# Kernel tuning notes

Measured on AMD Instinct MI355X. Metric: run time of the kernel, lower is better.

Reference implementation:

```python
import jax, jax.numpy as jnp
import numpy as np

V = 100000
E = 1600000
BN_EPS = 1e-5


def spmm(edge_index, vals, X):
    # X: (V, Cin, B); sparse L @ X via scatter-add. y[r] += w * X[c]
    rows, cols = edge_index[0], edge_index[1]
    return jnp.zeros_like(X).at[rows].add(vals[:, None, None] * X[cols])


def cheb_conv(x, edge_index, vals, w, b=None):
    # x: (B, Cin, V), w: (K, Cin, Cout) -> (B, Cout, V)
    K = w.shape[0]
    x0 = jnp.transpose(x, (2, 1, 0))  # (V, Cin, B)
    xs = [x0]
    if K > 1:
        x1 = spmm(edge_index, vals, x0)
        xs.append(x1)
        for _ in range(2, K):
            x2 = 2.0 * spmm(edge_index, vals, x1) - x0
            xs.append(x2)
            x0, x1 = x1, x2
    xk = jnp.stack(xs)  # (K, V, Cin, B)
    out = jnp.einsum('kvcb,kco->bov', xk, w)
    if b is not None:
        out = out + b[None, :, None]
    return out


def batch_norm(x, g, b):
    # training-mode BatchNorm1d on (B, C, V): stats over (B, V), biased var
    m = jnp.mean(x, axis=(0, 2), keepdims=True)
    v = jnp.var(x, axis=(0, 2), keepdims=True)
    return g[None, :, None] * (x - m) * jax.lax.rsqrt(v + BN_EPS) + b[None, :, None]


def setup_inputs() -> dict:
    key = jax.random.key(0)
    ks = jax.random.split(key, 8)
    x = jax.random.normal(ks[0], (4, 32, V), dtype=jnp.float32)
    edge_index = jax.random.randint(ks[1], (2, E), 0, V, dtype=jnp.int32)
    # small values keep the K=4 Chebyshev recursion well-scaled
    lap_vals = 0.1 * jax.random.normal(ks[2], (E,), dtype=jnp.float32)
    def w(k, K, cin, cout):
        s = 1.0 / np.sqrt(K * cin)
        return s * jax.random.normal(k, (K, cin, cout), dtype=jnp.float32)
    return {
        'x': x, 'edge_index': edge_index, 'lap_vals': lap_vals,
        'in_bn_g': jnp.ones((32,), jnp.float32), 'in_bn_b': jnp.zeros((32,), jnp.float32),
        'in_w': w(ks[3], 4, 32, 64), 'in_b': jnp.zeros((64,), jnp.float32),
        'h0_bn_g': jnp.ones((64,), jnp.float32), 'h0_bn_b': jnp.zeros((64,), jnp.float32),
        'h0_w': w(ks[4], 4, 64, 64), 'h0_b': jnp.zeros((64,), jnp.float32),
        'h1_bn_g': jnp.ones((64,), jnp.float32), 'h1_bn_b': jnp.zeros((64,), jnp.float32),
        'h1_w': w(ks[5], 4, 64, 32), 'h1_b': jnp.zeros((32,), jnp.float32),
    }


def reference(x, edge_index, lap_vals, in_bn_g, in_bn_b, in_w, in_b,
              h0_bn_g, h0_bn_b, h0_w, h0_b, h1_bn_g, h1_bn_b, h1_w, h1_b):
    xn = batch_norm(x, in_bn_g, in_bn_b)
    out = cheb_conv(xn, edge_index, lap_vals, in_w, in_b)
    # hidden layer 0
    out = jax.nn.relu(out)
    out = batch_norm(out, h0_bn_g, h0_bn_b)
    out = cheb_conv(out, edge_index, lap_vals, h0_w, h0_b)
    # hidden layer 1
    out = jax.nn.relu(out)
    out = batch_norm(out, h1_bn_g, h1_bn_b)
    out = cheb_conv(out, edge_index, lap_vals, h1_w, h1_b)
    # in_channels == out_channels -> Identity shortcut on the BN'ed input
    return jax.nn.relu(out + xn)
```

## Files before the change

### kernel.cpp

```cpp
#include <hip/hip_runtime.h>
#include <cstdint>
#include <cstddef>

#define VN 100000
#define EN 1600000
static constexpr float BN_EPS_F = 1e-5f;
static constexpr float INV_N = 1.0f / 400000.0f;

using short8 = __attribute__((ext_vector_type(8))) short;
using f32x4  = __attribute__((ext_vector_type(4))) float;

__device__ __forceinline__ float bf_lo(unsigned int p) {
  return __builtin_bit_cast(float, p << 16);
}
__device__ __forceinline__ float bf_hi(unsigned int p) {
  return __builtin_bit_cast(float, p & 0xffff0000u);
}
__device__ __forceinline__ float bf1(unsigned short u) {
  return __builtin_bit_cast(float, ((unsigned int)u) << 16);
}
__device__ __forceinline__ unsigned short f2bf(float f) {
  unsigned int x = __builtin_bit_cast(unsigned int, f);
  x += 0x7fffu + ((x >> 16) & 1u);
  return (unsigned short)(x >> 16);
}
__device__ __forceinline__ unsigned int pack2(float a, float b) {
  return (unsigned int)f2bf(a) | ((unsigned int)f2bf(b) << 16);
}

__global__ __launch_bounds__(256) void stats_x_kernel(const float* __restrict__ x,
                                                      float* __restrict__ stats) {
  const int p = blockIdx.x & 127;
  const int chunk = blockIdx.x >> 7;
  const int c = p & 31, b = p >> 5;
  const float* base = x + ((size_t)b * 32 + c) * VN + chunk * 12500;
  float s = 0.f, s2 = 0.f;
  for (int i = threadIdx.x; i < 12500; i += 256) {
    float v = base[i];
    s += v; s2 += v * v;
  }
  __shared__ float r1[256], r2[256];
  r1[threadIdx.x] = s; r2[threadIdx.x] = s2;
  __syncthreads();
  for (int off = 128; off > 0; off >>= 1) {
    if (threadIdx.x < off) {
      r1[threadIdx.x] += r1[threadIdx.x + off];
      r2[threadIdx.x] += r2[threadIdx.x + off];
    }
    __syncthreads();
  }
  if (threadIdx.x == 0) {
    atomicAdd(&stats[c], r1[0]);
    atomicAdd(&stats[64 + c], r2[0]);
  }
}

__global__ void finalize_stats_kernel(float* __restrict__ stats,
                                      const float* __restrict__ g,
                                      const float* __restrict__ beta, int C) {
  int c = threadIdx.x;
  if (c < C) {
    float m = stats[c] * INV_N;
    float var = stats[64 + c] * INV_N - m * m;
    float sc = g[c] * rsqrtf(var + BN_EPS_F);
    stats[128 + c] = sc;
    stats[192 + c] = beta[c] - m * sc;
  }
}

__global__ __launch_bounds__(128) void bn_transpose_kernel(const float* __restrict__ x,
                                                           const float* __restrict__ stats,
                                                           unsigned short* __restrict__ xn) {
  const int tid = threadIdx.x;
  const int b = tid >> 5, c = tid & 31;
  const int v0 = blockIdx.x * 64;
  const float sc = stats[128 + c], sh = stats[192 + c];
  const float* src = x + ((size_t)b * 32 + c) * VN;
  for (int i = 0; i < 64; i++) {
    int v = v0 + i;
    if (v < VN) xn[(size_t)v * 128 + tid] = f2bf(sc * src[v] + sh);
  }
}

__global__ __launch_bounds__(256) void pack_wb_kernel(const float* __restrict__ W,
                                                      unsigned short* __restrict__ Wb,
                                                      int Cin, int Cout) {
  const int i = blockIdx.x * 256 + threadIdx.x;
  const int KC = Cin >> 5, T = Cout >> 4;
  const int tot = 4 * KC * T * 512;
  if (i >= tot) return;
  const int j = i & 7;
  const int l = (i >> 3) & 63;
  const int rem = i >> 9;
  const int t = rem % T;
  const int kc = (rem / T) % KC;
  const int k = rem / (T * KC);
  const int c = kc * 32 + (l >> 4) * 8 + j;
  const int o = t * 16 + (l & 15);
  Wb[i] = f2bf(W[((size_t)k * Cin + c) * Cout + o]);
}

__global__ __launch_bounds__(256) void hist_kernel(const int* __restrict__ rows,
                                                   int* __restrict__ cnt) {
  int i = blockIdx.x * blockDim.x + threadIdx.x;
  const int stride = gridDim.x * blockDim.x;
  for (; i < EN; i += stride) atomicAdd(&cnt[rows[i]], 1);
}

__global__ __launch_bounds__(256) void scan1_kernel(const int* __restrict__ cnt,
                                                    int* __restrict__ rp,
                                                    int* __restrict__ chunkSums) {
  __shared__ int sh[256];
  const int t = threadIdx.x;
  const int base = blockIdx.x * 2048 + t * 8;
  int vals[8]; int tot = 0;
#pragma unroll
  for (int i = 0; i < 8; i++) {
    int idx = base + i;
    int v = (idx < VN) ? cnt[idx] : 0;
    vals[i] = v; tot += v;
  }
  sh[t] = tot;
  __syncthreads();
  for (int off = 1; off < 256; off <<= 1) {
    int v = (t >= off) ? sh[t - off] : 0;
    __syncthreads();
    sh[t] += v;
    __syncthreads();
  }
  int run = sh[t] - tot;
#pragma unroll
  for (int i = 0; i < 8; i++) {
    int idx = base + i;
    if (idx < VN) rp[idx] = run;
    run += vals[i];
  }
  if (t == 255) chunkSums[blockIdx.x] = sh[255];
}

__global__ void scan2_kernel(const int* __restrict__ chunkSums,
                             int* __restrict__ chunkOff,
                             int* __restrict__ rp, int nChunks) {
  if (threadIdx.x == 0 && blockIdx.x == 0) {
    int off = 0;
    for (int j = 0; j < nChunks; j++) { chunkOff[j] = off; off += chunkSums[j]; }
    rp[VN] = off;
  }
}

__global__ __launch_bounds__(256) void scan3_kernel(int* __restrict__ rp,
                                                    const int* __restrict__ chunkOff,
                                                    int* __restrict__ fill) {
  int i = blockIdx.x * 256 + threadIdx.x;
  if (i < VN) {
    int v = rp[i] + chunkOff[i >> 11];
    rp[i] = v;
    fill[i] = v;
  }
}

__global__ __launch_bounds__(256) void fill_kernel(const int* __restrict__ rows,
                                                   const int* __restrict__ cols,
                                                   const float* __restrict__ lap,
                                                   int* __restrict__ fill,
                                                   int* __restrict__ cols_s,
                                                   float* __restrict__ vals_s) {
  int i = blockIdx.x * blockDim.x + threadIdx.x;
  const int stride = gridDim.x * blockDim.x;
  for (; i < EN; i += stride) {
    int r = rows[i];
    int pos = atomicAdd(&fill[r], 1);
    cols_s[pos] = cols[i];
    vals_s[pos] = lap[i];
  }
}

template <int EPL, bool CHEB>
__global__ __launch_bounds__(256, 8) void spmm_kernel(const int* __restrict__ rp,
                                                   const int* __restrict__ cs,
                                                   const float* __restrict__ vs,
                                                   const unsigned short* __restrict__ X, int XS,
                                                   const unsigned short* __restrict__ P, int PS,
                                                   unsigned short* __restrict__ Y, int YS) {
  const int lane = threadIdx.x & 63;
  const int row = blockIdx.x * 4 + (threadIdx.x >> 6);
  const int start = rp[row], end = rp[row + 1];
  float acc[EPL];
#pragma unroll
  for (int j = 0; j < EPL; j++) acc[j] = 0.f;
  int e = start;
  for (; e + 4 <= end; e += 4) {
    const int c0 = cs[e], c1 = cs[e + 1], c2 = cs[e + 2], c3 = cs[e + 3];
    const float w0 = vs[e], w1 = vs[e + 1], w2 = vs[e + 2], w3 = vs[e + 3];
    if constexpr (EPL == 4) {
      const uint2 q0 = *reinterpret_cast<const uint2*>(X + (size_t)c0 * XS + lane * 4);
      const uint2 q1 = *reinterpret_cast<const uint2*>(X + (size_t)c1 * XS + lane * 4);
      const uint2 q2 = *reinterpret_cast<const uint2*>(X + (size_t)c2 * XS + lane * 4);
      const uint2 q3 = *reinterpret_cast<const uint2*>(X + (size_t)c3 * XS + lane * 4);
      acc[0] += w0 * bf_lo(q0.x) + w1 * bf_lo(q1.x) + w2 * bf_lo(q2.x) + w3 * bf_lo(q3.x);
      acc[1] += w0 * bf_hi(q0.x) + w1 * bf_hi(q1.x) + w2 * bf_hi(q2.x) + w3 * bf_hi(q3.x);
      acc[2] += w0 * bf_lo(q0.y) + w1 * bf_lo(q1.y) + w2 * bf_lo(q2.y) + w3 * bf_lo(q3.y);
      acc[3] += w0 * bf_hi(q0.y) + w1 * bf_hi(q1.y) + w2 * bf_hi(q2.y) + w3 * bf_hi(q3.y);
    } else {
      const unsigned int q0 = *reinterpret_cast<const unsigned int*>(X + (size_t)c0 * XS + lane * 2);
      const unsigned int q1 = *reinterpret_cast<const unsigned int*>(X + (size_t)c1 * XS + lane * 2);
      const unsigned int q2 = *reinterpret_cast<const unsigned int*>(X + (size_t)c2 * XS + lane * 2);
      const unsigned int q3 = *reinterpret_cast<const unsigned int*>(X + (size_t)c3 * XS + lane * 2);
      acc[0] += w0 * bf_lo(q0) + w1 * bf_lo(q1) + w2 * bf_lo(q2) + w3 * bf_lo(q3);
      acc[1] += w0 * bf_hi(q0) + w1 * bf_hi(q1) + w2 * bf_hi(q2) + w3 * bf_hi(q3);
    }
  }
  for (; e < end; e++) {
    const int c0 = cs[e];
    const float w0 = vs[e];
    if constexpr (EPL == 4) {
      const uint2 q0 = *reinterpret_cast<const uint2*>(X + (size_t)c0 * XS + lane * 4);
      acc[0] += w0 * bf_lo(q0.x);
      acc[1] += w0 * bf_hi(q0.x);
      acc[2] += w0 * bf_lo(q0.y);
      acc[3] += w0 * bf_hi(q0.y);
    } else {
      const unsigned int q0 = *reinterpret_cast<const unsigned int*>(X + (size_t)c0 * XS + lane * 2);
      acc[0] += w0 * bf_lo(q0);
      acc[1] += w0 * bf_hi(q0);
    }
  }
  if constexpr (EPL == 4) {
    if constexpr (CHEB) {
      const uint2 p = *reinterpret_cast<const uint2*>(P + (size_t)row * PS + lane * 4);
      acc[0] = 2.f * acc[0] - bf_lo(p.x);
      acc[1] = 2.f * acc[1] - bf_hi(p.x);
      acc[2] = 2.f * acc[2] - bf_lo(p.y);
      acc[3] = 2.f * acc[3] - bf_hi(p.y);
    }
    uint2 r;
    r.x = pack2(acc[0], acc[1]);
    r.y = pack2(acc[2], acc[3]);
    *reinterpret_cast<uint2*>(Y + (size_t)row * YS + lane * 4) = r;
  } else {
    if constexpr (CHEB) {
      const unsigned int p = *reinterpret_cast<const unsigned int*>(P + (size_t)row * PS + lane * 2);
      acc[0] = 2.f * acc[0] - bf_lo(p);
      acc[1] = 2.f * acc[1] - bf_hi(p);
    }
    *reinterpret_cast<unsigned int*>(Y + (size_t)row * YS + lane * 2) = pack2(acc[0], acc[1]);
  }
}

template <int Cin, int Cout, int X0S>
__global__ __launch_bounds__(256, 8) void fused_cheb_kernel(const int* __restrict__ rp,
                                                         const int* __restrict__ cs,
                                                         const float* __restrict__ vs,
                                                         const unsigned short* __restrict__ X0,
                                                         unsigned short* __restrict__ A,
                                                         const unsigned short* __restrict__ B,
                                                         const unsigned short* __restrict__ Wb,
                                                         const float* __restrict__ Bias) {
  constexpr int EPL = Cin * 4 / 64;
  constexpr int ROWSH = Cin * 4;
  __shared__ unsigned short t3s[4 * ROWSH];
  const int lane = threadIdx.x & 63;
  const int wv = threadIdx.x >> 6;
  const int row0 = blockIdx.x * 4;
  const int row = row0 + wv;

  float g[EPL];
#pragma unroll
  for (int j = 0; j < EPL; j++) g[j] = 0.f;
  const int start = rp[row], end = rp[row + 1];
  int e = start;
  for (; e + 4 <= end; e += 4) {
    const int c0 = cs[e], c1 = cs[e + 1], c2 = cs[e + 2], c3 = cs[e + 3];
    const float w0 = vs[e], w1 = vs[e + 1], w2 = vs[e + 2], w3 = vs[e + 3];
    if constexpr (EPL == 4) {
      const uint2 q0 = *reinterpret_cast<const uint2*>(B + (size_t)c0 * 256 + lane * 4);
      const uint2 q1 = *reinterpret_cast<const uint2*>(B + (size_t)c1 * 256 + lane * 4);
      const uint2 q2 = *reinterpret_cast<const uint2*>(B + (size_t)c2 * 256 + lane * 4);
      const uint2 q3 = *reinterpret_cast<const uint2*>(B + (size_t)c3 * 256 + lane * 4);
      g[0] += w0 * bf_lo(q0.x) + w1 * bf_lo(q1.x) + w2 * bf_lo(q2.x) + w3 * bf_lo(q3.x);
      g[1] += w0 * bf_hi(q0.x) + w1 * bf_hi(q1.x) + w2 * bf_hi(q2.x) + w3 * bf_hi(q3.x);
      g[2] += w0 * bf_lo(q0.y) + w1 * bf_lo(q1.y) + w2 * bf_lo(q2.y) + w3 * bf_lo(q3.y);
      g[3] += w0 * bf_hi(q0.y) + w1 * bf_hi(q1.y) + w2 * bf_hi(q2.y) + w3 * bf_hi(q3.y);
    } else {
      const unsigned int q0 = *reinterpret_cast<const unsigned int*>(B + (size_t)c0 * 256 + lane * 2);
      const unsigned int q1 = *reinterpret_cast<const unsigned int*>(B + (size_t)c1 * 256 + lane * 2);
      const unsigned int q2 = *reinterpret_cast<const unsigned int*>(B + (size_t)c2 * 256 + lane * 2);
      const unsigned int q3 = *reinterpret_cast<const unsigned int*>(B + (size_t)c3 * 256 + lane * 2);
      g[0] += w0 * bf_lo(q0) + w1 * bf_lo(q1) + w2 * bf_lo(q2) + w3 * bf_lo(q3);
      g[1] += w0 * bf_hi(q0) + w1 * bf_hi(q1) + w2 * bf_hi(q2) + w3 * bf_hi(q3);
    }
  }
  for (; e < end; e++) {
    const int c0 = cs[e];
    const float w0 = vs[e];
    if constexpr (EPL == 4) {
      const uint2 q0 = *reinterpret_cast<const uint2*>(B + (size_t)c0 * 256 + lane * 4);
      g[0] += w0 * bf_lo(q0.x);
      g[1] += w0 * bf_hi(q0.x);
      g[2] += w0 * bf_lo(q0.y);
      g[3] += w0 * bf_hi(q0.y);
    } else {
      const unsigned int q0 = *reinterpret_cast<const unsigned int*>(B + (size_t)c0 * 256 + lane * 2);
      g[0] += w0 * bf_lo(q0);
      g[1] += w0 * bf_hi(q0);
    }
  }
  {
    unsigned int* tw = reinterpret_cast<unsigned int*>(t3s + wv * ROWSH);
    if constexpr (EPL == 4) {
      const uint2 p = *reinterpret_cast<const uint2*>(A + (size_t)row * 256 + lane * 4);
      tw[lane * 2]     = pack2(2.f * g[0] - bf_lo(p.x), 2.f * g[1] - bf_hi(p.x));
      tw[lane * 2 + 1] = pack2(2.f * g[2] - bf_lo(p.y), 2.f * g[3] - bf_hi(p.y));
    } else {
      const unsigned int p = *reinterpret_cast<const unsigned int*>(A + (size_t)row * 256 + lane * 2);
      tw[lane] = pack2(2.f * g[0] - bf_lo(p), 2.f * g[1] - bf_hi(p));
    }
  }
  __syncthreads();

  constexpr int KC = Cin / 32;
  constexpr int T = Cout / 16;
  const int col = lane & 15, quad = lane >> 4;
  const int t = wv % T;
  const int ar = col >> 2, ab = col & 3;

  const unsigned short* xap[3];
  xap[0] = X0 + (size_t)(row0 + ar) * X0S + ab * Cin + quad * 8;
  xap[1] = A  + (size_t)(row0 + ar) * 256 + ab * Cin + quad * 8;
  xap[2] = B  + (size_t)(row0 + ar) * 256 + ab * Cin + quad * 8;
  const unsigned short* wb = Wb + (size_t)t * 512 + lane * 8;

  f32x4 acc = {0.f, 0.f, 0.f, 0.f};
#pragma unroll
  for (int k = 0; k < 3; k++) {
#pragma unroll
    for (int kc = 0; kc < KC; kc++) {
      const short8 af = *reinterpret_cast<const short8*>(xap[k] + kc * 32);
      const short8 bf = *reinterpret_cast<const short8*>(wb + (size_t)(k * KC + kc) * T * 512);
      acc = __builtin_amdgcn_mfma_f32_16x16x32_bf16(af, bf, acc, 0, 0, 0);
    }
  }
#pragma unroll
  for (int kc = 0; kc < KC; kc++) {
    const short8 af = *reinterpret_cast<const short8*>(&t3s[ar * ROWSH + ab * Cin + kc * 32 + quad * 8]);
    const short8 bf = *reinterpret_cast<const short8*>(wb + (size_t)(3 * KC + kc) * T * 512);
    acc = __builtin_amdgcn_mfma_f32_16x16x32_bf16(af, bf, acc, 0, 0, 0);
  }
  __syncthreads();

  if (T == 4 || wv < 2) {
    const int og = t * 16 + col;
    const float bs = Bias[og];
#pragma unroll
    for (int r = 0; r < 4; r++) {
      A[(size_t)(row0 + quad) * 256 + r * Cout + og] = f2bf(acc[r] + bs);
    }
  }
}

__global__ __launch_bounds__(256) void stats_out_kernel(const unsigned short* __restrict__ SRC,
                                                        float* __restrict__ stats) {
  const int tid = threadIdx.x;
  const int per = (VN + gridDim.x - 1) / gridDim.x;
  const int v0 = blockIdx.x * per;
  const int v1 = (v0 + per < VN) ? (v0 + per) : VN;
  float s = 0.f, s2 = 0.f;
  for (int v = v0; v < v1; v++) {
    float val = bf1(SRC[(size_t)v * 256 + tid]);
    val = fmaxf(val, 0.f);
    s += val; s2 += val * val;
  }
  __shared__ float r1[256], r2[256];
  r1[tid] = s; r2[tid] = s2;
  __syncthreads();
  if (tid < 64) {
    float a = r1[tid] + r1[tid + 64] + r1[tid + 128] + r1[tid + 192];
    float b = r2[tid] + r2[tid + 64] + r2[tid + 128] + r2[tid + 192];
    atomicAdd(&stats[tid], a);
    atomicAdd(&stats[64 + tid], b);
  }
}

__global__ __launch_bounds__(256) void bn_relu_kernel(const unsigned short* __restrict__ SRC,
                                                      const float* __restrict__ stats,
                                                      unsigned short* __restrict__ DST) {
  const int i = blockIdx.x * 256 + threadIdx.x;
  const int w = i & 63;
  const int o0 = (w & 15) * 4;
  const float4 sc4 = *reinterpret_cast<const float4*>(stats + 128 + o0);
  const float4 sh4 = *reinterpret_cast<const float4*>(stats + 192 + o0);
  const uint2 q = reinterpret_cast<const uint2*>(SRC)[i];
  float a = fmaxf(bf_lo(q.x), 0.f);
  float b = fmaxf(bf_hi(q.x), 0.f);
  float c = fmaxf(bf_lo(q.y), 0.f);
  float d = fmaxf(bf_hi(q.y), 0.f);
  uint2 r;
  r.x = pack2(a * sc4.x + sh4.x, b * sc4.y + sh4.y);
  r.y = pack2(c * sc4.z + sh4.z, d * sc4.w + sh4.w);
  reinterpret_cast<uint2*>(DST)[i] = r;
}

__global__ __launch_bounds__(256) void final_kernel(const unsigned short* __restrict__ SRC,
                                                    const unsigned short* __restrict__ xn,
                                                    float* __restrict__ out) {
  const int lane = threadIdx.x & 63;
  const int grp = threadIdx.x >> 6;
  const int v = blockIdx.x * 64 + lane;
  if (v >= VN) return;
  for (int ob = grp; ob < 128; ob += 4) {
    float val = bf1(SRC[(size_t)v * 256 + ob]) + bf1(xn[(size_t)v * 128 + ob]);
    val = fmaxf(val, 0.f);
    out[(size_t)ob * VN + v] = val;
  }
}

static constexpr size_t align_up(size_t x) { return (x + 255) & ~(size_t)255; }
static constexpr size_t OFF_RP    = 0;
static constexpr size_t OFF_FILL  = align_up(OFF_RP + (size_t)(VN + 1) * 4);
static constexpr size_t OFF_CHS   = align_up(OFF_FILL + (size_t)VN * 4);
static constexpr size_t OFF_CHO   = align_up(OFF_CHS + 256);
static constexpr size_t OFF_STATS = align_up(OFF_CHO + 256);
static constexpr size_t OFF_WP    = align_up(OFF_STATS + 1024);
static constexpr size_t OFF_CS    = align_up(OFF_WP + 32768 * 2);
static constexpr size_t OFF_VS    = align_up(OFF_CS + (size_t)EN * 4);
static constexpr size_t OFF_XN    = align_up(OFF_VS + (size_t)EN * 4);
static constexpr size_t OFF_XL    = align_up(OFF_XN + (size_t)VN * 128 * 2);
static constexpr size_t OFF_A     = align_up(OFF_XL + (size_t)VN * 256 * 2);
static constexpr size_t OFF_B     = align_up(OFF_A + (size_t)VN * 256 * 2);
static constexpr size_t OFF_END   = OFF_B + (size_t)VN * 256 * 2;

extern "C" void kernel_launch(void* const* d_in, const int* in_sizes, int n_in,
                              void* d_out, int out_size, void* d_ws, size_t ws_size,
                              hipStream_t stream) {
  if (ws_size < OFF_END) return;

  const float* x       = (const float*)d_in[0];
  const int*   rows    = (const int*)d_in[1];
  const int*   cols    = rows + EN;
  const float* lap     = (const float*)d_in[2];
  const float* in_bn_g = (const float*)d_in[3];
  const float* in_bn_b = (const float*)d_in[4];
  const float* in_w    = (const float*)d_in[5];
  const float* in_b    = (const float*)d_in[6];
  const float* h0_bn_g = (const float*)d_in[7];
  const float* h0_bn_b = (const float*)d_in[8];
  const float* h0_w    = (const float*)d_in[9];
  const float* h0_b    = (const float*)d_in[10];
  const float* h1_bn_g = (const float*)d_in[11];
  const float* h1_bn_b = (const float*)d_in[12];
  const float* h1_w    = (const float*)d_in[13];
  const float* h1_b    = (const float*)d_in[14];
  float* outp = (float*)d_out;

  char* ws = (char*)d_ws;
  int*   rp     = (int*)(ws + OFF_RP);
  int*   fill   = (int*)(ws + OFF_FILL);
  int*   chS    = (int*)(ws + OFF_CHS);
  int*   chO    = (int*)(ws + OFF_CHO);
  float* stats  = (float*)(ws + OFF_STATS);
  unsigned short* wbIn = (unsigned short*)(ws + OFF_WP);
  unsigned short* wbH0 = wbIn + 8192;
  unsigned short* wbH1 = wbH0 + 16384;
  int*   cs     = (int*)(ws + OFF_CS);
  float* vs     = (float*)(ws + OFF_VS);
  unsigned short* xn = (unsigned short*)(ws + OFF_XN);
  unsigned short* XL = (unsigned short*)(ws + OFF_XL);
  unsigned short* A  = (unsigned short*)(ws + OFF_A);
  unsigned short* B  = (unsigned short*)(ws + OFF_B);

  const int nChunks = (VN + 2047) / 2048;

  pack_wb_kernel<<<32, 256, 0, stream>>>(in_w, wbIn, 32, 64);
  pack_wb_kernel<<<64, 256, 0, stream>>>(h0_w, wbH0, 64, 64);
  pack_wb_kernel<<<32, 256, 0, stream>>>(h1_w, wbH1, 64, 32);

  hipMemsetAsync(stats, 0, 1024, stream);
  stats_x_kernel<<<1024, 256, 0, stream>>>(x, stats);
  finalize_stats_kernel<<<1, 64, 0, stream>>>(stats, in_bn_g, in_bn_b, 32);
  bn_transpose_kernel<<<1563, 128, 0, stream>>>(x, stats, xn);

  hipMemsetAsync(fill, 0, (size_t)VN * 4, stream);
  hist_kernel<<<2048, 256, 0, stream>>>(rows, fill);
  scan1_kernel<<<nChunks, 256, 0, stream>>>(fill, rp, chS);
  scan2_kernel<<<1, 64, 0, stream>>>(chS, chO, rp, nChunks);
  scan3_kernel<<<(VN + 255) / 256, 256, 0, stream>>>(rp, chO, fill);
  fill_kernel<<<2048, 256, 0, stream>>>(rows, cols, lap, fill, cs, vs);

  spmm_kernel<2, false><<<VN / 4, 256, 0, stream>>>(rp, cs, vs, xn, 128, nullptr, 0, A, 256);
  spmm_kernel<2, true ><<<VN / 4, 256, 0, stream>>>(rp, cs, vs, A, 256, xn, 128, B, 256);
  fused_cheb_kernel<32, 64, 128><<<VN / 4, 256, 0, stream>>>(rp, cs, vs, xn, A, B, wbIn, in_b);
  hipMemsetAsync(stats, 0, 1024, stream);
  stats_out_kernel<<<256, 256, 0, stream>>>(A, stats);
  finalize_stats_kernel<<<1, 64, 0, stream>>>(stats, h0_bn_g, h0_bn_b, 64);
  bn_relu_kernel<<<VN * 64 / 256, 256, 0, stream>>>(A, stats, XL);

  spmm_kernel<4, false><<<VN / 4, 256, 0, stream>>>(rp, cs, vs, XL, 256, nullptr, 0, A, 256);
  spmm_kernel<4, true ><<<VN / 4, 256, 0, stream>>>(rp, cs, vs, A, 256, XL, 256, B, 256);
  fused_cheb_kernel<64, 64, 256><<<VN / 4, 256, 0, stream>>>(rp, cs, vs, XL, A, B, wbH0, h0_b);
  hipMemsetAsync(stats, 0, 1024, stream);
  stats_out_kernel<<<256, 256, 0, stream>>>(A, stats);
  finalize_stats_kernel<<<1, 64, 0, stream>>>(stats, h1_bn_g, h1_bn_b, 64);
  bn_relu_kernel<<<VN * 64 / 256, 256, 0, stream>>>(A, stats, XL);

  spmm_kernel<4, false><<<VN / 4, 256, 0, stream>>>(rp, cs, vs, XL, 256, nullptr, 0, A, 256);
  spmm_kernel<4, true ><<<VN / 4, 256, 0, stream>>>(rp, cs, vs, A, 256, XL, 256, B, 256);
  fused_cheb_kernel<64, 32, 256><<<VN / 4, 256, 0, stream>>>(rp, cs, vs, XL, A, B, wbH1, h1_b);

  final_kernel<<<1563, 256, 0, stream>>>(A, xn, outp);
}
```

Measured before the change: 1.806 ms.

## Apply last-layer weights before propagation and use Clenshaw recurrence on narrower features

For the final Chebyshev layer (64 in, 32 out channels), a new MFMA kernel first projects the input with each of the four weight slices, giving four 32-channel tensors z0..z3. The Chebyshev sum is then evaluated with a Clenshaw backward recurrence, built from three sparse multiplies on 128-element rows instead of 256-element rows. The goal is to halve the bytes gathered per edge in the last layer's sparse passes, which are bound by memory traffic. In exchange it adds a separate GEMM pass, extra reads of the z tensors, and bf16 rounding at different points in the recurrence. The A and B buffers now have to sit next to each other in the workspace.

Measured after the change: 1.637 ms. -9.3%, faster.

```diff
diff --git a/kernel.cpp b/kernel.cpp
--- a/kernel.cpp
+++ b/kernel.cpp
@@ -175,12 +175,13 @@
   }
 }
 
-template <int EPL, bool CHEB>
+template <int EPL, int MODE>
 __global__ __launch_bounds__(256, 8) void spmm_kernel(const int* __restrict__ rp,
                                                    const int* __restrict__ cs,
                                                    const float* __restrict__ vs,
                                                    const unsigned short* __restrict__ X, int XS,
                                                    const unsigned short* __restrict__ P, int PS,
+                                                   const unsigned short* __restrict__ Q, int QS,
                                                    unsigned short* __restrict__ Y, int YS) {
   const int lane = threadIdx.x & 63;
   const int row = blockIdx.x * 4 + (threadIdx.x >> 6);
@@ -226,24 +227,40 @@
     }
   }
   if constexpr (EPL == 4) {
-    if constexpr (CHEB) {
+    float r0 = acc[0], r1 = acc[1], r2 = acc[2], r3 = acc[3];
+    if constexpr (MODE == 1) {
       const uint2 p = *reinterpret_cast<const uint2*>(P + (size_t)row * PS + lane * 4);
-      acc[0] = 2.f * acc[0] - bf_lo(p.x);
-      acc[1] = 2.f * acc[1] - bf_hi(p.x);
-      acc[2] = 2.f * acc[2] - bf_lo(p.y);
-      acc[3] = 2.f * acc[3] - bf_hi(p.y);
+      r0 = 2.f * r0 - bf_lo(p.x);
+      r1 = 2.f * r1 - bf_hi(p.x);
+      r2 = 2.f * r2 - bf_lo(p.y);
+      r3 = 2.f * r3 - bf_hi(p.y);
     }
     uint2 r;
-    r.x = pack2(acc[0], acc[1]);
-    r.y = pack2(acc[2], acc[3]);
+    r.x = pack2(r0, r1);
+    r.y = pack2(r2, r3);
     *reinterpret_cast<uint2*>(Y + (size_t)row * YS + lane * 4) = r;
   } else {
-    if constexpr (CHEB) {
+    float r0 = acc[0], r1 = acc[1];
+    if constexpr (MODE == 1) {
       const unsigned int p = *reinterpret_cast<const unsigned int*>(P + (size_t)row * PS + lane * 2);
-      acc[0] = 2.f * acc[0] - bf_lo(p);
-      acc[1] = 2.f * acc[1] - bf_hi(p);
-    }
-    *reinterpret_cast<unsigned int*>(Y + (size_t)row * YS + lane * 2) = pack2(acc[0], acc[1]);
+      r0 = 2.f * r0 - bf_lo(p);
+      r1 = 2.f * r1 - bf_hi(p);
+    } else if constexpr (MODE == 2) {
+      const unsigned int p = *reinterpret_cast<const unsigned int*>(P + (size_t)row * PS + lane * 2);
+      r0 = 2.f * r0 + bf_lo(p);
+      r1 = 2.f * r1 + bf_hi(p);
+    } else if constexpr (MODE == 3) {
+      const unsigned int p = *reinterpret_cast<const unsigned int*>(P + (size_t)row * PS + lane * 2);
+      const unsigned int qq = *reinterpret_cast<const unsigned int*>(Q + (size_t)row * QS + lane * 2);
+      r0 = 2.f * r0 - bf_lo(qq) + bf_lo(p);
+      r1 = 2.f * r1 - bf_hi(qq) + bf_hi(p);
+    } else if constexpr (MODE == 4) {
+      const unsigned int p = *reinterpret_cast<const unsigned int*>(P + (size_t)row * PS + lane * 2);
+      const unsigned int qq = *reinterpret_cast<const unsigned int*>(Q + (size_t)row * QS + lane * 2);
+      r0 = r0 - bf_lo(qq) + bf_lo(p);
+      r1 = r1 - bf_hi(qq) + bf_hi(p);
+    }
+    *reinterpret_cast<unsigned int*>(Y + (size_t)row * YS + lane * 2) = pack2(r0, r1);
   }
 }
 
@@ -358,6 +375,36 @@
   }
 }
 
+__global__ __launch_bounds__(256, 8) void gemm_z_kernel(const unsigned short* __restrict__ XL,
+                                                        const unsigned short* __restrict__ Wb,
+                                                        const float* __restrict__ Bias,
+                                                        unsigned short* __restrict__ Z) {
+  const int lane = threadIdx.x & 63;
+  const int wv = threadIdx.x >> 6;
+  const int row0 = blockIdx.x * 4;
+  const int col = lane & 15, quad = lane >> 4;
+  const int ar = col >> 2, ab = col & 3;
+  const unsigned short* xa = XL + (size_t)(row0 + ar) * 256 + ab * 64 + quad * 8;
+  const unsigned short* wb = Wb + (size_t)wv * 4 * 512 + lane * 8;
+  unsigned short* zr = Z + (size_t)wv * VN * 128;
+#pragma unroll
+  for (int t = 0; t < 2; t++) {
+    f32x4 acc = {0.f, 0.f, 0.f, 0.f};
+#pragma unroll
+    for (int kc = 0; kc < 2; kc++) {
+      const short8 af = *reinterpret_cast<const short8*>(xa + kc * 32);
+      const short8 bf = *reinterpret_cast<const short8*>(wb + (size_t)(kc * 2 + t) * 512);
+      acc = __builtin_amdgcn_mfma_f32_16x16x32_bf16(af, bf, acc, 0, 0, 0);
+    }
+    const int og = t * 16 + col;
+    const float bs = (wv == 0) ? Bias[og] : 0.f;
+#pragma unroll
+    for (int r = 0; r < 4; r++) {
+      zr[(size_t)(row0 + quad) * 128 + r * 32 + og] = f2bf(acc[r] + bs);
+    }
+  }
+}
+
 __global__ __launch_bounds__(256) void stats_out_kernel(const unsigned short* __restrict__ SRC,
                                                         float* __restrict__ stats) {
   const int tid = threadIdx.x;
@@ -408,7 +455,7 @@
   const int v = blockIdx.x * 64 + lane;
   if (v >= VN) return;
   for (int ob = grp; ob < 128; ob += 4) {
-    float val = bf1(SRC[(size_t)v * 256 + ob]) + bf1(xn[(size_t)v * 128 + ob]);
+    float val = bf1(SRC[(size_t)v * 128 + ob]) + bf1(xn[(size_t)v * 128 + ob]);
     val = fmaxf(val, 0.f);
     out[(size_t)ob * VN + v] = val;
   }
@@ -428,6 +475,7 @@
 static constexpr size_t OFF_A     = align_up(OFF_XL + (size_t)VN * 256 * 2);
 static constexpr size_t OFF_B     = align_up(OFF_A + (size_t)VN * 256 * 2);
 static constexpr size_t OFF_END   = OFF_B + (size_t)VN * 256 * 2;
+static_assert(OFF_B == OFF_A + (size_t)VN * 256 * 2, "A|B must be contiguous for Clenshaw z layout");
 
 extern "C" void kernel_launch(void* const* d_in, const int* in_sizes, int n_in,
                               void* d_out, int out_size, void* d_ws, size_t ws_size,
@@ -486,25 +534,32 @@
   scan3_kernel<<<(VN + 255) / 256, 256, 0, stream>>>(rp, chO, fill);
   fill_kernel<<<2048, 256, 0, stream>>>(rows, cols, lap, fill, cs, vs);
 
-  spmm_kernel<2, false><<<VN / 4, 256, 0, stream>>>(rp, cs, vs, xn, 128, nullptr, 0, A, 256);
-  spmm_kernel<2, true ><<<VN / 4, 256, 0, stream>>>(rp, cs, vs, A, 256, xn, 128, B, 256);
+  spmm_kernel<2, 0><<<VN / 4, 256, 0, stream>>>(rp, cs, vs, xn, 128, nullptr, 0, nullptr, 0, A, 256);
+  spmm_kernel<2, 1><<<VN / 4, 256, 0, stream>>>(rp, cs, vs, A, 256, xn, 128, nullptr, 0, B, 256);
   fused_cheb_kernel<32, 64, 128><<<VN / 4, 256, 0, stream>>>(rp, cs, vs, xn, A, B, wbIn, in_b);
   hipMemsetAsync(stats, 0, 1024, stream);
   stats_out_kernel<<<256, 256, 0, stream>>>(A, stats);
   finalize_stats_kernel<<<1, 64, 0, stream>>>(stats, h0_bn_g, h0_bn_b, 64);
   bn_relu_kernel<<<VN * 64 / 256, 256, 0, stream>>>(A, stats, XL);
 
-  spmm_kernel<4, false><<<VN / 4, 256, 0, stream>>>(rp, cs, vs, XL, 256, nullptr, 0, A, 256);
-  spmm_kernel<4, true ><<<VN / 4, 256, 0, stream>>>(rp, cs, vs, A, 256, XL, 256, B, 256);
+  spmm_kernel<4, 0><<<VN / 4, 256, 0, stream>>>(rp, cs, vs, XL, 256, nullptr, 0, nullptr, 0, A, 256);
+  spmm_kernel<4, 1><<<VN / 4, 256, 0, stream>>>(rp, cs, vs, A, 256, XL, 256, nullptr, 0, B, 256);
   fused_cheb_kernel<64, 64, 256><<<VN / 4, 256, 0, stream>>>(rp, cs, vs, XL, A, B, wbH0, h0_b);
   hipMemsetAsync(stats, 0, 1024, stream);
   stats_out_kernel<<<256, 256, 0, stream>>>(A, stats);
   finalize_stats_kernel<<<1, 64, 0, stream>>>(stats, h1_bn_g, h1_bn_b, 64);
   bn_relu_kernel<<<VN * 64 / 256, 256, 0, stream>>>(A, stats, XL);
 
-  spmm_kernel<4, false><<<VN / 4, 256, 0, stream>>>(rp, cs, vs, XL, 256, nullptr, 0, A, 256);
-  spmm_kernel<4, true ><<<VN / 4, 256, 0, stream>>>(rp, cs, vs, A, 256, XL, 256, B, 256);
-  fused_cheb_kernel<64, 32, 256><<<VN / 4, 256, 0, stream>>>(rp, cs, vs, XL, A, B, wbH1, h1_b);
-
-  final_kernel<<<1563, 256, 0, stream>>>(A, xn, outp);
-}
+  {
+    unsigned short* Z  = A;
+    unsigned short* z0 = Z;
+    unsigned short* z1 = Z + (size_t)VN * 128;
+    unsigned short* z2 = Z + (size_t)VN * 256;
+    unsigned short* z3 = Z + (size_t)VN * 384;
+    gemm_z_kernel<<<VN / 4, 256, 0, stream>>>(XL, wbH1, h1_b, Z);
+    spmm_kernel<2, 2><<<VN / 4, 256, 0, stream>>>(rp, cs, vs, z3, 128, z2, 128, nullptr, 0, z2, 128);
+    spmm_kernel<2, 3><<<VN / 4, 256, 0, stream>>>(rp, cs, vs, z2, 128, z1, 128, z3, 128, z1, 128);
+    spmm_kernel<2, 4><<<VN / 4, 256, 0, stream>>>(rp, cs, vs, z1, 128, z0, 128, z2, 128, z0, 128);
+    final_kernel<<<1563, 256, 0, stream>>>(z0, xn, outp);
+  }
+}
```
